# Kernel tuning notes

Measured on AMD Instinct MI355X. Metric: run time of the kernel, lower is better.

Reference implementation:

```python
import jax, jax.numpy as jnp
import numpy as np
from jax import lax

START, STOP, NTAGS = 18, 19, 20
NEG = -10000.0
V, E, H, L = 100000, 300, 512, 512  # vocab, embed_dim, per-direction hidden, seq_len


def setup_inputs() -> dict:
    key = jax.random.key(0)
    ks = jax.random.split(key, 16)
    f = lambda k, s: jax.random.normal(k, s, dtype=jnp.float32) * 0.05
    trans = jax.random.normal(ks[14], (NTAGS, NTAGS), dtype=jnp.float32)
    trans = trans.at[START, :].set(NEG).at[:, STOP].set(NEG)
    return {
        "sentence": jax.random.randint(ks[0], (L,), 0, V),
        "embed_table": f(ks[1], (V, E)),
        "w_ih_f": f(ks[2], (4 * H, E)), "w_hh_f": f(ks[3], (4 * H, H)),
        "b_ih_f": f(ks[4], (4 * H,)), "b_hh_f": f(ks[5], (4 * H,)),
        "w_ih_b": f(ks[6], (4 * H, E)), "w_hh_b": f(ks[7], (4 * H, H)),
        "b_ih_b": f(ks[8], (4 * H,)), "b_hh_b": f(ks[9], (4 * H,)),
        "h0": f(ks[10], (2, H)), "c0": f(ks[11], (2, H)),
        "w_out": f(ks[12], (NTAGS, 2 * H)), "b_out": f(ks[13], (NTAGS,)),
        "transitions": trans,
    }


def _lstm_dir(x, wih, whh, bih, bhh, h0, c0, reverse):
    # x: [L, E]; PyTorch gate order i, f, g, o
    b = bih + bhh
    def step(carry, xt):
        h, c = carry
        g = xt @ wih.T + h @ whh.T + b  # [4H]
        i, fg, gg, o = jnp.split(g, 4)
        c = jax.nn.sigmoid(fg) * c + jax.nn.sigmoid(i) * jnp.tanh(gg)
        h = jax.nn.sigmoid(o) * jnp.tanh(c)
        return (h, c), h
    _, hs = lax.scan(step, (h0, c0), x, reverse=reverse)
    return hs  # [L, H] in time order


def _lstm_feats(sentence, embed_table, w_ih_f, w_hh_f, b_ih_f, b_hh_f,
                w_ih_b, w_hh_b, b_ih_b, b_hh_b, h0, c0, w_out, b_out):
    x = embed_table[sentence]  # [L, E]
    hf = _lstm_dir(x, w_ih_f, w_hh_f, b_ih_f, b_hh_f, h0[0], c0[0], False)
    hb = _lstm_dir(x, w_ih_b, w_hh_b, b_ih_b, b_hh_b, h0[1], c0[1], True)
    h = jnp.concatenate([hf, hb], axis=-1)  # [L, 2H]
    return h @ w_out.T + b_out  # [L, NTAGS]


def reference(sentence, embed_table, w_ih_f, w_hh_f, b_ih_f, b_hh_f,
              w_ih_b, w_hh_b, b_ih_b, b_hh_b, h0, c0, w_out, b_out, transitions):
    feats = _lstm_feats(sentence, embed_table, w_ih_f, w_hh_f, b_ih_f, b_hh_f,
                        w_ih_b, w_hh_b, b_ih_b, b_hh_b, h0, c0, w_out, b_out)
    init = jnp.full((NTAGS,), NEG, dtype=feats.dtype).at[START].set(0.0)

    def vstep(fv, feat):
        scores = fv[None, :] + transitions  # [next_tag, prev_tag]
        bptr = jnp.argmax(scores, axis=1)
        return jnp.max(scores, axis=1) + feat, bptr

    fv, bptrs = lax.scan(vstep, init, feats)  # bptrs: [L, NTAGS]
    terminal = fv + transitions[STOP]
    best = jnp.argmax(terminal)

    def back(tag, bp):
        # tag is the best tag at step t; bp maps tag_t -> tag_{t-1}
        return bp[tag], tag

    _, path = lax.scan(back, best, bptrs, reverse=True)  # [L] in time order
    return path
```

## Files before the change

### kernel.cpp

```cpp
#include <hip/hip_runtime.h>
#include <math.h>

typedef unsigned long long u64;
typedef unsigned int u32;

#define L 512
#define E 300
#define H 512
#define G4H 2048
#define NTAGS 20
#define START_TAG 18
#define STOP_TAG 19

#define KC 100

#define OFF_XW    0u
#define OFF_HIST  8388608u
#define OFF_HBUF  10485760u
#define OFF_FEATS 10502144u

__global__ __launch_bounds__(256) void k1_xw(
    const int* __restrict__ sentence, const float* __restrict__ embed,
    const float* __restrict__ wih_f, const float* __restrict__ wih_b,
    const float* __restrict__ bih_f, const float* __restrict__ bhh_f,
    const float* __restrict__ bih_b, const float* __restrict__ bhh_b,
    float* __restrict__ xw) {
    __shared__ float wST[KC][68];
    __shared__ float xST[KC][68];
    __shared__ int   sT[64];

    const int tid = threadIdx.x;
    const int tx = tid & 15;
    const int ty = tid >> 4;
    const int n_base = blockIdx.x * 64;
    const int t_base = blockIdx.y * 64;
    const int dir = blockIdx.z;
    const float* wih = dir ? wih_b : wih_f;
    const float* bih = dir ? bih_b : bih_f;
    const float* bhh = dir ? bhh_b : bhh_f;

    if (tid < 64) sT[tid] = sentence[t_base + tid];
    __syncthreads();

    float acc[4][4];
#pragma unroll
    for (int i = 0; i < 4; ++i)
#pragma unroll
        for (int j = 0; j < 4; ++j) acc[i][j] = 0.f;

    for (int kc = 0; kc < E; kc += KC) {
#pragma unroll
        for (int i = 0; i < 25; ++i) {
            int idx = i * 256 + tid;
            int row = idx / KC, col = idx % KC;
            wST[col][row] = wih[(size_t)(n_base + row) * E + kc + col];
        }
#pragma unroll
        for (int i = 0; i < 25; ++i) {
            int idx = i * 256 + tid;
            int trow = idx / KC, col = idx % KC;
            xST[col][trow] = embed[(size_t)sT[trow] * E + kc + col];
        }
        __syncthreads();

#pragma unroll 4
        for (int k = 0; k < KC; ++k) {
            float4 wv4 = *(const float4*)&wST[k][ty * 4];
            float4 xv4 = *(const float4*)&xST[k][tx * 4];
            float wv[4] = {wv4.x, wv4.y, wv4.z, wv4.w};
            float xv[4] = {xv4.x, xv4.y, xv4.z, xv4.w};
#pragma unroll
            for (int i = 0; i < 4; ++i)
#pragma unroll
                for (int j = 0; j < 4; ++j)
                    acc[i][j] = fmaf(wv[i], xv[j], acc[i][j]);
        }
        __syncthreads();
    }

#pragma unroll
    for (int i = 0; i < 4; ++i) {
        int n = n_base + ty * 4 + i;
        float b = bih[n] + bhh[n];
        int u = n & (H - 1), g = n >> 9;
        int pos = (u >> 4) * 64 + ((u & 15) >> 1) * 8 + g * 2 + (u & 1);
#pragma unroll
        for (int j = 0; j < 4; ++j) {
            int t = t_base + tx * 4 + j;
            xw[((size_t)(dir * L) + t) * G4H + pos] = acc[i][j] + b;
        }
    }
}

__global__ __launch_bounds__(512) void k2_lstm(
    const float* __restrict__ whh_f, const float* __restrict__ whh_b,
    const float* __restrict__ h0, const float* __restrict__ c0,
    const float* __restrict__ xw, float* __restrict__ hist,
    u64* __restrict__ hbuf) {
    const int bid = blockIdx.x;
    const int dir = bid >> 5;
    const int wg  = bid & 31;
    const int tid = threadIdx.x;
    const int wv  = tid >> 6;
    const int l   = tid & 63;
    const int j   = l & 7;
    const int q   = l >> 3;
    const int g   = j >> 1;
    const int p   = j & 1;
    const int u0  = wg * 16;
    const int unit = u0 + 2 * wv + p;
    const int grow = g * H + unit;

    const float* whh = dir ? whh_b : whh_f;
    float* histd = hist + (size_t)dir * L * H;
    u64* hb = hbuf + dir * 1024;

    float w[64];
    {
        const float* wp = whh + (size_t)grow * H + q * 64;
#pragma unroll
        for (int i = 0; i < 64; i += 4) {
            float4 v = *(const float4*)(wp + i);
            w[i] = v.x; w[i+1] = v.y; w[i+2] = v.z; w[i+3] = v.w;
        }
    }

    __shared__ float hstage[2][8 * 68];

    float c = 0.f;
    if (l < 2) c = c0[dir * H + u0 + 2 * wv + l];

    for (int s = 1; s <= L; ++s) {
        const int t = dir ? (L - s) : (s - 1);
        const int par = s & 1;

        float xwv = 0.f;
        if (l < 8)
            xwv = xw[((size_t)(dir * L) + t) * G4H + wg * 64 + wv * 8 + j];

        float hval;
        if (s == 1) {
            hval = h0[dir * H + tid];
        } else {
            u64* slot = hb + ((s - 1) & 1) * 512 + tid;
            u64 u;
            while (((u = __hip_atomic_load(slot, __ATOMIC_RELAXED,
                                           __HIP_MEMORY_SCOPE_AGENT)) >> 32)
                   != (u32)(s - 1))
                __builtin_amdgcn_s_sleep(1);
            hval = __uint_as_float((u32)u);
        }
        hstage[par][(tid >> 6) * 68 + (tid & 63)] = hval;
        __syncthreads();

        float acc = 0.f;
        const int base = q * 68;
#pragma unroll
        for (int i = 0; i < 64; i += 4) {
            float4 h4 = *(__shared__ float4*)&hstage[par][base + i];
            acc = fmaf(w[i], h4.x, fmaf(w[i+1], h4.y,
                  fmaf(w[i+2], h4.z, fmaf(w[i+3], h4.w, acc))));
        }
        acc += __shfl_xor(acc, 8);
        acc += __shfl_xor(acc, 16);
        acc += __shfl_xor(acc, 32);

        float pre = acc + xwv;
        float a2 = (g == 2) ? 2.f * pre : pre;
        float sg = 1.f / (1.f + __expf(-a2));
        float vg = (g == 2) ? (2.f * sg - 1.f) : sg;

        float gi = __shfl(vg, p);
        float gf = __shfl(vg, 2 + p);
        float gg = __shfl(vg, 4 + p);
        float go = __shfl(vg, 6 + p);
        float hout = 0.f;
        if (l < 2) {
            c = gf * c + gi * gg;
            float th = 2.f / (1.f + __expf(-2.f * c)) - 1.f;
            hout = go * th;
        }
        float h1 = __shfl(hout, 1);
        if (l == 0) {
            u64* bb = hb + par * 512 + u0 + 2 * wv;
            u64 e0 = ((u64)(u32)s << 32) | (u64)__float_as_uint(hout);
            u64 e1 = ((u64)(u32)s << 32) | (u64)__float_as_uint(h1);
            __hip_atomic_store(bb,     e0, __ATOMIC_RELAXED, __HIP_MEMORY_SCOPE_AGENT);
            __hip_atomic_store(bb + 1, e1, __ATOMIC_RELAXED, __HIP_MEMORY_SCOPE_AGENT);
        }
        if (l < 2)
            histd[(size_t)t * H + u0 + 2 * wv + l] = hout;
    }
}

__global__ void k3_feats(const float* __restrict__ hist,
                         const float* __restrict__ wout,
                         const float* __restrict__ bout,
                         float* __restrict__ feats) {
    int t = blockIdx.x;
    int tid = threadIdx.x;
    int tag = tid >> 4;
    int part = tid & 15;
    const float* h0p = hist + (size_t)t * H;
    const float* h1p = hist + (size_t)L * H + (size_t)t * H;
    int j0 = part * 64;
    float acc = 0.f;
    for (int jj = 0; jj < 64; jj += 4) {
        int j = j0 + jj;
        float4 w4 = *(const float4*)(wout + (size_t)tag * (2 * H) + j);
        float4 h4 = (j < H) ? *(const float4*)(h0p + j)
                            : *(const float4*)(h1p + (j - H));
        acc = fmaf(w4.x, h4.x, fmaf(w4.y, h4.y,
              fmaf(w4.z, h4.z, fmaf(w4.w, h4.w, acc))));
    }
    acc += __shfl_xor(acc, 8, 16);
    acc += __shfl_xor(acc, 4, 16);
    acc += __shfl_xor(acc, 2, 16);
    acc += __shfl_xor(acc, 1, 16);
    if (part == 0) feats[(size_t)t * NTAGS + tag] = acc + bout[tag];
}

__global__ void k4_viterbi(const float* __restrict__ feats,
                           const float* __restrict__ trans,
                           int* __restrict__ out) {
    __shared__ unsigned char bp[L * NTAGS];
    int lane = threadIdx.x;
    bool act = lane < NTAGS;

    float trl[NTAGS];
#pragma unroll
    for (int p = 0; p < NTAGS; ++p)
        trl[p] = act ? trans[lane * NTAGS + p] : -1.0e30f;

    float fv = (lane == START_TAG) ? 0.f : -10000.f;
    float nf = act ? feats[lane] : 0.f;

    for (int t = 0; t < L; ++t) {
        float f = nf;
        if (act && t + 1 < L) nf = feats[(size_t)(t + 1) * NTAGS + lane];
        float tv[NTAGS];
        int   ti[NTAGS];
#pragma unroll
        for (int p = 0; p < NTAGS; ++p) {
            tv[p] = __shfl(fv, p) + trl[p];
            ti[p] = p;
        }
#pragma unroll
        for (int p = 0; p < 4; ++p) {
            bool take = (tv[p + 16] > tv[p]) ||
                        (tv[p + 16] == tv[p] && ti[p + 16] < ti[p]);
            if (take) { tv[p] = tv[p + 16]; ti[p] = ti[p + 16]; }
        }
#pragma unroll
        for (int w = 8; w >= 1; w >>= 1)
#pragma unroll
            for (int p = 0; p < 16; ++p) if (p < w) {
                bool take = (tv[p + w] > tv[p]) ||
                            (tv[p + w] == tv[p] && ti[p + w] < ti[p]);
                if (take) { tv[p] = tv[p + w]; ti[p] = ti[p + w]; }
            }
        fv = tv[0] + f;
        if (act) bp[t * NTAGS + lane] = (unsigned char)ti[0];
    }

    float ts = act ? fv + trans[STOP_TAG * NTAGS + lane] : -1.0e30f;
    int bi = lane;
#pragma unroll
    for (int off = 32; off; off >>= 1) {
        float ov = __shfl_down(ts, off);
        int   oi = __shfl_down(bi, off);
        if (ov > ts) { ts = ov; bi = oi; }
    }
    if (lane == 0) {
        int tag = bi;
        out[L - 1] = tag;
        for (int t = L - 1; t >= 1; --t) {
            tag = bp[t * NTAGS + tag];
            out[t - 1] = tag;
        }
    }
}

extern "C" void kernel_launch(void* const* d_in, const int* in_sizes, int n_in,
                              void* d_out, int out_size, void* d_ws, size_t ws_size,
                              hipStream_t stream) {
    const int*   sentence = (const int*)d_in[0];
    const float* embed    = (const float*)d_in[1];
    const float* wih_f    = (const float*)d_in[2];
    const float* whh_f    = (const float*)d_in[3];
    const float* bih_f    = (const float*)d_in[4];
    const float* bhh_f    = (const float*)d_in[5];
    const float* wih_b    = (const float*)d_in[6];
    const float* whh_b    = (const float*)d_in[7];
    const float* bih_b    = (const float*)d_in[8];
    const float* bhh_b    = (const float*)d_in[9];
    const float* h0       = (const float*)d_in[10];
    const float* c0       = (const float*)d_in[11];
    const float* wout     = (const float*)d_in[12];
    const float* bout     = (const float*)d_in[13];
    const float* trans    = (const float*)d_in[14];
    int* out = (int*)d_out;

    char* ws = (char*)d_ws;
    float* xw    = (float*)(ws + OFF_XW);
    float* hist  = (float*)(ws + OFF_HIST);
    float* feats = (float*)(ws + OFF_FEATS);
    u64*   hbuf  = (u64*)(ws + OFF_HBUF);

    k1_xw<<<dim3(32, 8, 2), 256, 0, stream>>>(sentence, embed, wih_f, wih_b,
                                              bih_f, bhh_f, bih_b, bhh_b, xw);
    k2_lstm<<<64, 512, 0, stream>>>(whh_f, whh_b, h0, c0, xw, hist, hbuf);
    k3_feats<<<L, 320, 0, stream>>>(hist, wout, bout, feats);
    k4_viterbi<<<1, 64, 0, stream>>>(feats, trans, out);
}
```

Baseline: 1.705 ms.

## Restructure LSTM recurrence to broadcast h via readlane and reduce partials in LDS

Each wave now owns a 64-column slice of h and computes partial dot products for all 64 gate rows of the workgroup, broadcasting h elements with readlane instead of staging h through shared memory before the matvec. Partial sums go through a single LDS exchange followed by cross-lane shuffles, and the xw gate layout is reordered to match the new lane-to-gate mapping. The spin-wait sleep is also removed to cut polling latency. The cost is many scalar readlane operations per step and busier polling on the global flags.

```diff
diff --git a/kernel.cpp b/kernel.cpp
--- a/kernel.cpp
+++ b/kernel.cpp
@@ -83,7 +83,7 @@
         int n = n_base + ty * 4 + i;
         float b = bih[n] + bhh[n];
         int u = n & (H - 1), g = n >> 9;
-        int pos = (u >> 4) * 64 + ((u & 15) >> 1) * 8 + g * 2 + (u & 1);
+        int pos = (u >> 4) * 64 + (u & 15) * 4 + g;
 #pragma unroll
         for (int j = 0; j < 4; ++j) {
             int t = t_base + tx * 4 + j;
@@ -103,13 +103,9 @@
     const int tid = threadIdx.x;
     const int wv  = tid >> 6;
     const int l   = tid & 63;
-    const int j   = l & 7;
-    const int q   = l >> 3;
-    const int g   = j >> 1;
-    const int p   = j & 1;
-    const int u0  = wg * 16;
-    const int unit = u0 + 2 * wv + p;
-    const int grow = g * H + unit;
+    const int jj  = l >> 2;
+    const int g   = l & 3;
+    const int grow = g * H + wg * 16 + jj;
 
     const float* whh = dir ? whh_b : whh_f;
     float* histd = hist + (size_t)dir * L * H;
@@ -117,7 +113,7 @@
 
     float w[64];
     {
-        const float* wp = whh + (size_t)grow * H + q * 64;
+        const float* wp = whh + (size_t)grow * H + wv * 64;
 #pragma unroll
         for (int i = 0; i < 64; i += 4) {
             float4 v = *(const float4*)(wp + i);
@@ -125,10 +121,10 @@
         }
     }
 
-    __shared__ float hstage[2][8 * 68];
+    __shared__ float pbuf[2][8][68];
 
     float c = 0.f;
-    if (l < 2) c = c0[dir * H + u0 + 2 * wv + l];
+    if (l == 0 || l == 4) c = c0[dir * H + wg * 16 + 2 * wv + (l >> 2)];
 
     for (int s = 1; s <= L; ++s) {
         const int t = dir ? (L - s) : (s - 1);
@@ -136,7 +132,7 @@
 
         float xwv = 0.f;
         if (l < 8)
-            xwv = xw[((size_t)(dir * L) + t) * G4H + wg * 64 + wv * 8 + j];
+            xwv = xw[((size_t)(dir * L) + t) * G4H + wg * 64 + wv * 8 + l];
 
         float hval;
         if (s == 1) {
@@ -146,50 +142,51 @@
             u64 u;
             while (((u = __hip_atomic_load(slot, __ATOMIC_RELAXED,
                                            __HIP_MEMORY_SCOPE_AGENT)) >> 32)
-                   != (u32)(s - 1))
-                __builtin_amdgcn_s_sleep(1);
+                   != (u32)(s - 1)) { }
             hval = __uint_as_float((u32)u);
         }
-        hstage[par][(tid >> 6) * 68 + (tid & 63)] = hval;
+
+        float a0 = 0.f, a1 = 0.f, a2 = 0.f, a3 = 0.f;
+#pragma unroll
+        for (int i = 0; i < 64; i += 4) {
+            float h0v = __uint_as_float((u32)__builtin_amdgcn_readlane(
+                            (int)__float_as_uint(hval), i));
+            float h1v = __uint_as_float((u32)__builtin_amdgcn_readlane(
+                            (int)__float_as_uint(hval), i + 1));
+            float h2v = __uint_as_float((u32)__builtin_amdgcn_readlane(
+                            (int)__float_as_uint(hval), i + 2));
+            float h3v = __uint_as_float((u32)__builtin_amdgcn_readlane(
+                            (int)__float_as_uint(hval), i + 3));
+            a0 = fmaf(w[i],     h0v, a0);
+            a1 = fmaf(w[i + 1], h1v, a1);
+            a2 = fmaf(w[i + 2], h2v, a2);
+            a3 = fmaf(w[i + 3], h3v, a3);
+        }
+        pbuf[par][wv][l] = (a0 + a1) + (a2 + a3);
         __syncthreads();
 
-        float acc = 0.f;
-        const int base = q * 68;
-#pragma unroll
-        for (int i = 0; i < 64; i += 4) {
-            float4 h4 = *(__shared__ float4*)&hstage[par][base + i];
-            acc = fmaf(w[i], h4.x, fmaf(w[i+1], h4.y,
-                  fmaf(w[i+2], h4.z, fmaf(w[i+3], h4.w, acc))));
-        }
-        acc += __shfl_xor(acc, 8);
-        acc += __shfl_xor(acc, 16);
-        acc += __shfl_xor(acc, 32);
-
-        float pre = acc + xwv;
-        float a2 = (g == 2) ? 2.f * pre : pre;
-        float sg = 1.f / (1.f + __expf(-a2));
+        float part = pbuf[par][l >> 3][8 * wv + (l & 7)];
+        part += __shfl_xor(part, 8);
+        part += __shfl_xor(part, 16);
+        part += __shfl_xor(part, 32);
+        float pre = part + xwv;
+        float aa = (g == 2) ? 2.f * pre : pre;
+        float sg = 1.f / (1.f + __expf(-aa));
         float vg = (g == 2) ? (2.f * sg - 1.f) : sg;
-
-        float gi = __shfl(vg, p);
-        float gf = __shfl(vg, 2 + p);
-        float gg = __shfl(vg, 4 + p);
-        float go = __shfl(vg, 6 + p);
-        float hout = 0.f;
-        if (l < 2) {
+        float gi = __shfl(vg, (l & 4));
+        float gf = __shfl(vg, (l & 4) + 1);
+        float gg = __shfl(vg, (l & 4) + 2);
+        float go = __shfl(vg, (l & 4) + 3);
+        if (l == 0 || l == 4) {
             c = gf * c + gi * gg;
             float th = 2.f / (1.f + __expf(-2.f * c)) - 1.f;
-            hout = go * th;
-        }
-        float h1 = __shfl(hout, 1);
-        if (l == 0) {
-            u64* bb = hb + par * 512 + u0 + 2 * wv;
-            u64 e0 = ((u64)(u32)s << 32) | (u64)__float_as_uint(hout);
-            u64 e1 = ((u64)(u32)s << 32) | (u64)__float_as_uint(h1);
-            __hip_atomic_store(bb,     e0, __ATOMIC_RELAXED, __HIP_MEMORY_SCOPE_AGENT);
-            __hip_atomic_store(bb + 1, e1, __ATOMIC_RELAXED, __HIP_MEMORY_SCOPE_AGENT);
-        }
-        if (l < 2)
-            histd[(size_t)t * H + u0 + 2 * wv + l] = hout;
+            float hout = go * th;
+            int u = wg * 16 + 2 * wv + (l >> 2);
+            u64 e = ((u64)(u32)s << 32) | (u64)__float_as_uint(hout);
+            __hip_atomic_store(hb + par * 512 + u, e,
+                               __ATOMIC_RELAXED, __HIP_MEMORY_SCOPE_AGENT);
+            histd[(size_t)t * H + u] = hout;
+        }
     }
 }
 
```

Result: faster. 1.605 ms (-5.9%).
